# Kernel optimization log

Measured on AMD Instinct MI355X. Metric: run time of the kernel, lower is better.

Reference implementation:

```python
import jax, jax.numpy as jnp
import numpy as np

H, W, NUM_BUCKETS, NUM_LOOPS = 512, 512, 6, 4
N_DET, N_SAMPLES, BATCH = 4096, 128, 4


def setup_inputs() -> dict:
    key = jax.random.key(0)
    k1, k2, k3, k4 = jax.random.split(key, 4)
    det_indices = jax.random.uniform(k1, (N_DET, N_SAMPLES, 2), dtype=jnp.float32)
    det_indices = det_indices * jnp.array([W - 1, H - 1], jnp.float32)  # (x, y) coords
    refinement = jax.random.normal(k2, (BATCH, 2 * NUM_BUCKETS, H, W), dtype=jnp.float32)
    sampling = jax.random.uniform(k3, (N_SAMPLES,), dtype=jnp.float32)
    b = jax.random.randint(k4, (N_DET,), 0, BATCH, dtype=jnp.int64 if jax.config.jax_enable_x64 else jnp.int32)
    return {"det_indices": det_indices, "refinement": refinement, "sampling": sampling,
            "b": b, "num_loops": NUM_LOOPS, "num_buckets": NUM_BUCKETS, "height": H, "width": W}


def _bucket_weight(idx_f, base):
    # triangular weight: 1 - |idx - base|, zero outside unit distance; detached in torch
    d = jnp.abs(idx_f - base)
    return jax.lax.stop_gradient(jnp.where(d > 1.0, 0.0, 1.0 - d))


def reference(det_indices, refinement, sampling, b, num_loops, num_buckets, height, width):
    base = sampling * num_buckets               # [S]
    base_int = jnp.floor(base).astype(jnp.int32)
    det = det_indices
    for _ in range(num_loops):
        det = jnp.round(jax.lax.stop_gradient(det))
        det = jnp.stack([jnp.clip(det[..., 0], 0, width - 1),
                         jnp.clip(det[..., 1], 0, height - 1)], -1)
        idx = det.astype(jnp.int32)
        xi, yi = idx[..., 0], idx[..., 1]       # [N, S]
        responses = jnp.zeros_like(det)
        for off in (-1, 0, 1):
            bi = (base_int + off) % num_buckets                       # [S]
            w = _bucket_weight((base_int + off).astype(base.dtype), base)  # [S]
            bckt = jnp.stack([bi * 2, bi * 2 + 1], -1)                # [S, 2] channel pairs
            # gather -> [N, S, 2]
            cur = refinement[b[:, None, None], bckt[None, :, :], yi[..., None], xi[..., None]]
            responses = responses + cur * w[None, :, None]
        det = det + responses
    return det
```

## Files before the change

### kernel.cpp

```cpp
#include <hip/hip_runtime.h>

#define HREF   512
#define WREF   512
#define NBUCK  6
#define NLOOP  4
#define NDET   4096
#define NSAMP  128
#define BATCH  4
#define PLANE  (HREF * WREF)
#define NCHAN  (2 * NBUCK)
#define RECSZ  16

__global__ __launch_bounds__(256) void CPN_transpose_kernel(
    const float* __restrict__ ref, float* __restrict__ ws)
{
    const int t = blockIdx.x * blockDim.x + threadIdx.x;
    const int b = t >> 18;
    const int p = t & (PLANE - 1);

    const float* src = ref + (size_t)b * NCHAN * PLANE + p;
    float* dst = ws + ((size_t)t << 4);

    float v[NCHAN + 2];
    #pragma unroll
    for (int c = 0; c < NCHAN; ++c) v[c] = src[(size_t)c << 18];
    v[12] = v[0];
    v[13] = v[1];

    *(float4*)(dst + 0)  = make_float4(v[0], v[1], v[2],  v[3]);
    *(float4*)(dst + 4)  = make_float4(v[4], v[5], v[6],  v[7]);
    *(float4*)(dst + 8)  = make_float4(v[8], v[9], v[10], v[11]);
    *(float2*)(dst + 12) = make_float2(v[12], v[13]);
}

__global__ __launch_bounds__(256) void CPN_4492535791617_kernel(
    const float* __restrict__ det_in,
    const float* __restrict__ ws,
    const float* __restrict__ sampling,
    const int*   __restrict__ bsel,
    float*       __restrict__ out)
{
    const int tid = blockIdx.x * blockDim.x + threadIdx.x;
    const int s = tid & (NSAMP - 1);
    const int d = tid >> 7;

    float2 det = ((const float2*)det_in)[tid];
    const int bb = bsel[d];

    const float base = sampling[s] * (float)NBUCK;
    const float bf   = floorf(base);
    const float frac = base - bf;
    const float w0   = 1.0f - frac;
    const float w1   = frac;
    int bi = (int)bf;
    if (bi >= NBUCK) bi -= NBUCK;
    if (bi < 0)      bi  = 0;

    const float* slab_bi = ws + ((size_t)bb << 22) + 2 * bi;

    #pragma unroll
    for (int l = 0; l < NLOOP; ++l) {
        float x = rintf(det.x);
        float y = rintf(det.y);
        x = fminf(fmaxf(x, 0.0f), (float)(WREF - 1));
        y = fminf(fmaxf(y, 0.0f), (float)(HREF - 1));
        const int p = (int)y * WREF + (int)x;

        const float4 q = *(const float4*)(slab_bi + ((size_t)p << 4));

        det.x = x + (w0 * q.x + w1 * q.z);
        det.y = y + (w0 * q.y + w1 * q.w);
    }

    ((float2*)out)[tid] = det;
}

__global__ __launch_bounds__(256) void CPN_fallback_kernel(
    const float* __restrict__ det_in,
    const float* __restrict__ refinement,
    const float* __restrict__ sampling,
    const int*   __restrict__ bsel,
    float*       __restrict__ out)
{
    const int tid = blockIdx.x * blockDim.x + threadIdx.x;
    const int s = tid & (NSAMP - 1);
    const int d = tid >> 7;

    float2 det = ((const float2*)det_in)[tid];
    const int bb = bsel[d];

    const float base = sampling[s] * (float)NBUCK;
    const float bf   = floorf(base);
    const float frac = base - bf;
    const float w0   = 1.0f - frac;
    const float w1   = frac;
    int bi = (int)bf;
    if (bi >= NBUCK) bi -= NBUCK;
    if (bi < 0)      bi  = 0;
    int bj = bi + 1; if (bj >= NBUCK) bj -= NBUCK;

    const size_t plane = (size_t)PLANE;
    const float* slab = refinement + (size_t)bb * NCHAN * plane;
    const float* c0 = slab + (size_t)(2 * bi)     * plane;
    const float* c1 = slab + (size_t)(2 * bi + 1) * plane;
    const float* c2 = slab + (size_t)(2 * bj)     * plane;
    const float* c3 = slab + (size_t)(2 * bj + 1) * plane;

    #pragma unroll
    for (int l = 0; l < NLOOP; ++l) {
        float x = rintf(det.x);
        float y = rintf(det.y);
        x = fminf(fmaxf(x, 0.0f), (float)(WREF - 1));
        y = fminf(fmaxf(y, 0.0f), (float)(HREF - 1));
        const int p = (int)y * WREF + (int)x;
        det.x = x + (w0 * c0[p] + w1 * c2[p]);
        det.y = y + (w0 * c1[p] + w1 * c3[p]);
    }

    ((float2*)out)[tid] = det;
}

extern "C" void kernel_launch(void* const* d_in, const int* in_sizes, int n_in,
                              void* d_out, int out_size, void* d_ws, size_t ws_size,
                              hipStream_t stream) {
    const float* det_indices = (const float*)d_in[0];
    const float* refinement  = (const float*)d_in[1];
    const float* sampling    = (const float*)d_in[2];
    const int*   b           = (const int*)  d_in[3];
    float* out = (float*)d_out;

    const size_t need = (size_t)BATCH * PLANE * RECSZ * sizeof(float);

    const int total = NDET * NSAMP;
    const int block = 256;
    const int grid  = total / block;

    if (ws_size >= need) {
        float* ws = (float*)d_ws;
        const int tp_total = BATCH * PLANE;
        CPN_transpose_kernel<<<tp_total / block, block, 0, stream>>>(refinement, ws);
        CPN_4492535791617_kernel<<<grid, block, 0, stream>>>(
            det_indices, ws, sampling, b, out);
    } else {
        CPN_fallback_kernel<<<grid, block, 0, stream>>>(
            det_indices, refinement, sampling, b, out);
    }
}
```

Baseline: 147.6 us.

## Drop transpose pre-pass and gather directly from planar refinement

Removes the kernel that repacked the refinement tensor into per-pixel interleaved records and always runs the direct-gather kernel on the original channel-planar layout. This removes a full read-and-write pass over the refinement data each call. In exchange, each refinement step now issues four separate scattered loads into different planes instead of one vector load, so more cache lines are touched per gather. The batch index is also made wave-uniform with readfirstlane, since a wavefront stays within one detection.

```diff
diff --git a/kernel.cpp b/kernel.cpp
--- a/kernel.cpp
+++ b/kernel.cpp
@@ -9,73 +9,8 @@
 #define BATCH  4
 #define PLANE  (HREF * WREF)
 #define NCHAN  (2 * NBUCK)
-#define RECSZ  16
-
-__global__ __launch_bounds__(256) void CPN_transpose_kernel(
-    const float* __restrict__ ref, float* __restrict__ ws)
-{
-    const int t = blockIdx.x * blockDim.x + threadIdx.x;
-    const int b = t >> 18;
-    const int p = t & (PLANE - 1);
-
-    const float* src = ref + (size_t)b * NCHAN * PLANE + p;
-    float* dst = ws + ((size_t)t << 4);
-
-    float v[NCHAN + 2];
-    #pragma unroll
-    for (int c = 0; c < NCHAN; ++c) v[c] = src[(size_t)c << 18];
-    v[12] = v[0];
-    v[13] = v[1];
-
-    *(float4*)(dst + 0)  = make_float4(v[0], v[1], v[2],  v[3]);
-    *(float4*)(dst + 4)  = make_float4(v[4], v[5], v[6],  v[7]);
-    *(float4*)(dst + 8)  = make_float4(v[8], v[9], v[10], v[11]);
-    *(float2*)(dst + 12) = make_float2(v[12], v[13]);
-}
 
 __global__ __launch_bounds__(256) void CPN_4492535791617_kernel(
-    const float* __restrict__ det_in,
-    const float* __restrict__ ws,
-    const float* __restrict__ sampling,
-    const int*   __restrict__ bsel,
-    float*       __restrict__ out)
-{
-    const int tid = blockIdx.x * blockDim.x + threadIdx.x;
-    const int s = tid & (NSAMP - 1);
-    const int d = tid >> 7;
-
-    float2 det = ((const float2*)det_in)[tid];
-    const int bb = bsel[d];
-
-    const float base = sampling[s] * (float)NBUCK;
-    const float bf   = floorf(base);
-    const float frac = base - bf;
-    const float w0   = 1.0f - frac;
-    const float w1   = frac;
-    int bi = (int)bf;
-    if (bi >= NBUCK) bi -= NBUCK;
-    if (bi < 0)      bi  = 0;
-
-    const float* slab_bi = ws + ((size_t)bb << 22) + 2 * bi;
-
-    #pragma unroll
-    for (int l = 0; l < NLOOP; ++l) {
-        float x = rintf(det.x);
-        float y = rintf(det.y);
-        x = fminf(fmaxf(x, 0.0f), (float)(WREF - 1));
-        y = fminf(fmaxf(y, 0.0f), (float)(HREF - 1));
-        const int p = (int)y * WREF + (int)x;
-
-        const float4 q = *(const float4*)(slab_bi + ((size_t)p << 4));
-
-        det.x = x + (w0 * q.x + w1 * q.z);
-        det.y = y + (w0 * q.y + w1 * q.w);
-    }
-
-    ((float2*)out)[tid] = det;
-}
-
-__global__ __launch_bounds__(256) void CPN_fallback_kernel(
     const float* __restrict__ det_in,
     const float* __restrict__ refinement,
     const float* __restrict__ sampling,
@@ -87,7 +22,7 @@
     const int d = tid >> 7;
 
     float2 det = ((const float2*)det_in)[tid];
-    const int bb = bsel[d];
+    const int bb = __builtin_amdgcn_readfirstlane(bsel[d]);
 
     const float base = sampling[s] * (float)NBUCK;
     const float bf   = floorf(base);
@@ -113,8 +48,14 @@
         x = fminf(fmaxf(x, 0.0f), (float)(WREF - 1));
         y = fminf(fmaxf(y, 0.0f), (float)(HREF - 1));
         const int p = (int)y * WREF + (int)x;
-        det.x = x + (w0 * c0[p] + w1 * c2[p]);
-        det.y = y + (w0 * c1[p] + w1 * c3[p]);
+
+        const float g0 = c0[p];
+        const float g1 = c1[p];
+        const float g2 = c2[p];
+        const float g3 = c3[p];
+
+        det.x = x + (w0 * g0 + w1 * g2);
+        det.y = y + (w0 * g1 + w1 * g3);
     }
 
     ((float2*)out)[tid] = det;
@@ -129,20 +70,10 @@
     const int*   b           = (const int*)  d_in[3];
     float* out = (float*)d_out;
 
-    const size_t need = (size_t)BATCH * PLANE * RECSZ * sizeof(float);
-
     const int total = NDET * NSAMP;
     const int block = 256;
     const int grid  = total / block;
 
-    if (ws_size >= need) {
-        float* ws = (float*)d_ws;
-        const int tp_total = BATCH * PLANE;
-        CPN_transpose_kernel<<<tp_total / block, block, 0, stream>>>(refinement, ws);
-        CPN_4492535791617_kernel<<<grid, block, 0, stream>>>(
-            det_indices, ws, sampling, b, out);
-    } else {
-        CPN_fallback_kernel<<<grid, block, 0, stream>>>(
-            det_indices, refinement, sampling, b, out);
-    }
+    CPN_4492535791617_kernel<<<grid, block, 0, stream>>>(
+        det_indices, refinement, sampling, b, out);
 }
```

Measured after the change: 224.1 us. 1.52x slower.
